# Optimization experiments

Hardware: AMD Instinct MI355X
Metric: run time of the kernel (lower is better)

## Reference

```python
import jax, jax.numpy as jnp
import numpy as np


def setup_inputs() -> dict:
    key = jax.random.key(0)
    k1, k2, k3, k4 = jax.random.split(key, 4)
    B, S, IN, OUT = 4, 2048, 4096, 11008
    x = jax.random.normal(k1, (B, S, IN), dtype=jnp.float32)
    # fp8-quantized weight values (simulated as small-magnitude floats stored in the param)
    weight = jax.random.normal(k2, (OUT, IN), dtype=jnp.float32)
    # per-output-channel dequant scale
    weight_scale = jax.random.uniform(k3, (OUT,), dtype=jnp.float32)
    bias = jax.random.normal(k4, (OUT,), dtype=jnp.float32)
    return {"x": x, "weight": weight, "weight_scale": weight_scale, "bias": bias}


def reference(x, weight, weight_scale, bias):
    # _dequant_weight: cast quantized weight to float32, broadcast per-row scale
    # (scale unsqueezed on trailing dims -> shape [out, 1]), multiply, cast to
    # compute dtype (x.dtype).
    compute_dtype = x.dtype
    q = weight.astype(jnp.float32)
    w = (q * weight_scale.astype(jnp.float32)[:, None]).astype(compute_dtype)  # [out, in]
    b = bias.astype(compute_dtype)
    # F.linear: y = x @ w.T + b
    y = jnp.einsum("bsi,oi->bso", x, w) + b
    return y
```

## Files before the change

### kernel.cpp

```cpp
#include <hip/hip_runtime.h>

#define M_DIM 8192
#define N_DIM 11008
#define K_DIM 4096
#define BM 256
#define BN 256
#define BK 64
#define NT (K_DIM / BK)
#define NIT (NT / 2)
#define TM (M_DIM / BM)
#define TN (N_DIM / BN)
#define NWG (TM * TN)

typedef __attribute__((ext_vector_type(8))) short bf16x8;
typedef __attribute__((ext_vector_type(8))) unsigned short u16x8;
typedef __attribute__((ext_vector_type(4))) float f32x4;

__device__ __forceinline__ unsigned short f2bf(float f) {
  union { float f; unsigned u; } v; v.f = f;
  unsigned r = v.u + 0x7FFFu + ((v.u >> 16) & 1u);
  return (unsigned short)(r >> 16);
}

__device__ __forceinline__ void gload_lds16(const unsigned short* g, unsigned short* l) {
  __builtin_amdgcn_global_load_lds(
      (const __attribute__((address_space(1))) void*)g,
      (__attribute__((address_space(3))) void*)l, 16, 0, 0);
}

__device__ __forceinline__ int swz(int b) { return b ^ (((b >> 7) & 7) << 4); }

#define BAR() asm volatile("s_barrier" ::: "memory")

__global__ void cvt_x_kernel(const float* __restrict__ in, unsigned short* __restrict__ o) {
  size_t i = (size_t)blockIdx.x * 256 + threadIdx.x;
  const float4* p = (const float4*)in + i * 2;
  float4 f0 = p[0], f1 = p[1];
  u16x8 v;
  v[0] = f2bf(f0.x); v[1] = f2bf(f0.y); v[2] = f2bf(f0.z); v[3] = f2bf(f0.w);
  v[4] = f2bf(f1.x); v[5] = f2bf(f1.y); v[6] = f2bf(f1.z); v[7] = f2bf(f1.w);
  *((u16x8*)o + i) = v;
}

__global__ void cvt_w_kernel(const float* __restrict__ in, const float* __restrict__ sc,
                             unsigned short* __restrict__ o) {
  size_t i = (size_t)blockIdx.x * 256 + threadIdx.x;
  float s = sc[i >> 9];
  const float4* p = (const float4*)in + i * 2;
  float4 f0 = p[0], f1 = p[1];
  u16x8 v;
  v[0] = f2bf(f0.x * s); v[1] = f2bf(f0.y * s); v[2] = f2bf(f0.z * s); v[3] = f2bf(f0.w * s);
  v[4] = f2bf(f1.x * s); v[5] = f2bf(f1.y * s); v[6] = f2bf(f1.z * s); v[7] = f2bf(f1.w * s);
  *((u16x8*)o + i) = v;
}

__launch_bounds__(512, 2)
__global__ void gemm_kernel(const unsigned short* __restrict__ xb,
                            const unsigned short* __restrict__ wb,
                            const float* __restrict__ bias,
                            float* __restrict__ out) {
  __shared__ unsigned short As[2][2][8192];
  __shared__ unsigned short Bs[2][2][8192];

  const int tid = threadIdx.x;
  const int lane = tid & 63;
  const int wave = tid >> 6;
  const int wr = wave >> 2;
  const int wc = wave & 3;

  int orig = blockIdx.x;
  int wg = (orig & 7) * (NWG / 8) + (orig >> 3);
  int bx = wg / TM;
  int by = wg % TM;
  const int rowBase = by * BM;
  const int colBase = bx * BN;

  f32x4 acc[8][4] = {};

  const int fr = lane & 15;
  const int q16 = (lane >> 4) * 16;

  float bias_v[4];
#pragma unroll
  for (int n = 0; n < 4; ++n)
    bias_v[n] = bias[colBase + wc * 64 + n * 16 + fr];

  const int L0 = tid * 16, L1 = L0 + 8192;
  const int S0 = swz(L0), S1 = swz(L1);
  const int sr0 = S0 >> 7, sc0_ = (S0 & 127) >> 1;
  const int sr1 = S1 >> 7, sc1_ = (S1 & 127) >> 1;

  auto stageA = [&](int kt, int half) {
    const unsigned short* src =
        xb + (size_t)(rowBase + half * 128) * K_DIM + (size_t)kt * BK;
    unsigned short* dst = &As[kt & 1][half][0];
    gload_lds16(src + (size_t)sr0 * K_DIM + sc0_, dst + (L0 >> 1));
    gload_lds16(src + (size_t)sr1 * K_DIM + sc1_, dst + (L1 >> 1));
  };
  auto stageB = [&](int kt, int half) {
    const unsigned short* src =
        wb + (size_t)(colBase + half * 128) * K_DIM + (size_t)kt * BK;
    unsigned short* dst = &Bs[kt & 1][half][0];
    gload_lds16(src + (size_t)sr0 * K_DIM + sc0_, dst + (L0 >> 1));
    gload_lds16(src + (size_t)sr1 * K_DIM + sc1_, dst + (L1 >> 1));
  };

  bf16x8 aF[8], bLo[4], bHi[4];

  auto rdA = [&](int d, int qm) {
    const char* Ab = (const char*)&As[d][wr][0];
#pragma unroll
    for (int mi = 0; mi < 4; ++mi)
#pragma unroll
      for (int ks = 0; ks < 2; ++ks) {
        int b = (qm * 64 + mi * 16 + fr) * 128 + ks * 64 + q16;
        aF[mi * 2 + ks] = *(const bf16x8*)(Ab + swz(b));
      }
  };
  auto rdB = [&](int d, int qn, bf16x8* bf) {
    const char* Bb = (const char*)&Bs[d][wc >> 1][0];
#pragma unroll
    for (int nj = 0; nj < 2; ++nj)
#pragma unroll
      for (int ks = 0; ks < 2; ++ks) {
        int b = ((wc & 1) * 64 + qn * 32 + nj * 16 + fr) * 128 + ks * 64 + q16;
        bf[nj * 2 + ks] = *(const bf16x8*)(Bb + swz(b));
      }
  };
  auto mma = [&](int qm, int qn, const bf16x8* bf) {
    __builtin_amdgcn_s_setprio(1);
#pragma unroll
    for (int mi = 0; mi < 4; ++mi)
#pragma unroll
      for (int nj = 0; nj < 2; ++nj)
#pragma unroll
        for (int ks = 0; ks < 2; ++ks)
          acc[qm * 4 + mi][qn * 2 + nj] = __builtin_amdgcn_mfma_f32_16x16x32_bf16(
              aF[mi * 2 + ks], bf[nj * 2 + ks], acc[qm * 4 + mi][qn * 2 + nj], 0, 0, 0);
    __builtin_amdgcn_s_setprio(0);
  };

  auto iter = [&](int a, bool f) {
    const int b = a + 1;
    rdA(0, 0); rdB(0, 0, bLo);
    stageA(b, 0);
    BAR(); mma(0, 0, bLo); BAR();
    rdB(0, 1, bHi);
    stageA(b, 1);
    BAR(); mma(0, 1, bHi); BAR();
    rdA(0, 1);
    if (f) stageB(a + 2, 0);
    BAR();
    mma(1, 1, bHi);
    if (f) stageB(a + 2, 1);
    mma(1, 0, bLo);
    if (f) { asm volatile("s_waitcnt vmcnt(4)" ::: "memory"); }
    else   { asm volatile("s_waitcnt vmcnt(0)" ::: "memory"); }
    BAR();
    rdA(1, 0); rdB(1, 0, bLo);
    if (f) stageA(a + 2, 0);
    BAR(); mma(0, 0, bLo); BAR();
    rdB(1, 1, bHi);
    if (f) stageA(a + 2, 1);
    BAR(); mma(0, 1, bHi); BAR();
    rdA(1, 1);
    if (f) stageB(a + 3, 0);
    BAR();
    mma(1, 1, bHi);
    if (f) stageB(a + 3, 1);
    mma(1, 0, bLo);
    if (f) { asm volatile("s_waitcnt vmcnt(4)" ::: "memory"); }
    BAR();
  };

  stageB(0, 0); stageB(0, 1);
  stageA(0, 0); stageA(0, 1);
  stageB(1, 0); stageB(1, 1);
  asm volatile("s_waitcnt vmcnt(4)" ::: "memory");
  BAR();

  for (int it = 0; it < NIT - 1; ++it) iter(2 * it, true);
  iter(NT - 2, false);

  const int r0 = (lane >> 4) * 4;
#pragma unroll
  for (int m = 0; m < 8; ++m) {
#pragma unroll
    for (int r = 0; r < 4; ++r) {
      size_t row = (size_t)(rowBase + wr * 128 + m * 16 + r0 + r);
      float* po = out + row * N_DIM + colBase + wc * 64 + fr;
#pragma unroll
      for (int n = 0; n < 4; ++n)
        po[n * 16] = acc[m][n][r] + bias_v[n];
    }
  }
}

extern "C" void kernel_launch(void* const* d_in, const int* in_sizes, int n_in,
                              void* d_out, int out_size, void* d_ws, size_t ws_size,
                              hipStream_t stream) {
  const float* x = (const float*)d_in[0];
  const float* w = (const float*)d_in[1];
  const float* sc = (const float*)d_in[2];
  const float* bi = (const float*)d_in[3];
  float* out = (float*)d_out;

  const size_t xe = (size_t)M_DIM * K_DIM;
  const size_t we = (size_t)N_DIM * K_DIM;
  unsigned short* xb = (unsigned short*)d_ws;
  unsigned short* wb = xb + xe;

  cvt_x_kernel<<<(unsigned)(xe / 8 / 256), 256, 0, stream>>>(x, xb);
  cvt_w_kernel<<<(unsigned)(we / 8 / 256), 256, 0, stream>>>(w, sc, wb);
  gemm_kernel<<<NWG, 512, 0, stream>>>(xb, wb, bi, out);
}
```

Measured before the change: 919.0 us.

## Software-pipeline LDS fragment reads with double register buffers across MFMA phases

Restructures the GEMM main loop so LDS fragment loads for the next quadrant are issued into separate register buffers (aP/aQ, bX/bY/bH) while MFMAs on the previous fragments run. Explicit lgkmcnt waits and sched_barrier fences pin the interleaving, and the last quadrant's MFMA is deferred into the next macro step. Global-to-LDS staging is redistributed with vmcnt(2) waits. The aim is to hide LDS read latency behind matrix work and drop some barriers, at the cost of more VGPR pressure under a 2-waves-per-SIMD launch bound and fragile hand-tuned wait counts.

```diff
diff --git a/kernel.cpp b/kernel.cpp
--- a/kernel.cpp
+++ b/kernel.cpp
@@ -7,7 +7,7 @@
 #define BN 256
 #define BK 64
 #define NT (K_DIM / BK)
-#define NIT (NT / 2)
+#define NMAC (NT / 2)
 #define TM (M_DIM / BM)
 #define TN (N_DIM / BN)
 #define NWG (TM * TN)
@@ -31,6 +31,7 @@
 __device__ __forceinline__ int swz(int b) { return b ^ (((b >> 7) & 7) << 4); }
 
 #define BAR() asm volatile("s_barrier" ::: "memory")
+#define SB0() __builtin_amdgcn_sched_barrier(0)
 
 __global__ void cvt_x_kernel(const float* __restrict__ in, unsigned short* __restrict__ o) {
   size_t i = (size_t)blockIdx.x * 256 + threadIdx.x;
@@ -105,29 +106,29 @@
     gload_lds16(src + (size_t)sr1 * K_DIM + sc1_, dst + (L1 >> 1));
   };
 
-  bf16x8 aF[8], bLo[4], bHi[4];
-
-  auto rdA = [&](int d, int qm) {
+  bf16x8 aP[8], aQ[8], bX[4], bY[4], bH[4];
+
+  auto rdA = [&](int d, int qm, bf16x8* dst) {
     const char* Ab = (const char*)&As[d][wr][0];
 #pragma unroll
     for (int mi = 0; mi < 4; ++mi)
 #pragma unroll
       for (int ks = 0; ks < 2; ++ks) {
         int b = (qm * 64 + mi * 16 + fr) * 128 + ks * 64 + q16;
-        aF[mi * 2 + ks] = *(const bf16x8*)(Ab + swz(b));
+        dst[mi * 2 + ks] = *(const bf16x8*)(Ab + swz(b));
       }
   };
-  auto rdB = [&](int d, int qn, bf16x8* bf) {
+  auto rdB = [&](int d, int qn, bf16x8* dst) {
     const char* Bb = (const char*)&Bs[d][wc >> 1][0];
 #pragma unroll
     for (int nj = 0; nj < 2; ++nj)
 #pragma unroll
       for (int ks = 0; ks < 2; ++ks) {
         int b = ((wc & 1) * 64 + qn * 32 + nj * 16 + fr) * 128 + ks * 64 + q16;
-        bf[nj * 2 + ks] = *(const bf16x8*)(Bb + swz(b));
+        dst[nj * 2 + ks] = *(const bf16x8*)(Bb + swz(b));
       }
   };
-  auto mma = [&](int qm, int qn, const bf16x8* bf) {
+  auto mma = [&](int qm, int qn, const bf16x8* A, const bf16x8* B) {
     __builtin_amdgcn_s_setprio(1);
 #pragma unroll
     for (int mi = 0; mi < 4; ++mi)
@@ -136,51 +137,69 @@
 #pragma unroll
         for (int ks = 0; ks < 2; ++ks)
           acc[qm * 4 + mi][qn * 2 + nj] = __builtin_amdgcn_mfma_f32_16x16x32_bf16(
-              aF[mi * 2 + ks], bf[nj * 2 + ks], acc[qm * 4 + mi][qn * 2 + nj], 0, 0, 0);
+              A[mi * 2 + ks], B[nj * 2 + ks], acc[qm * 4 + mi][qn * 2 + nj], 0, 0, 0);
     __builtin_amdgcn_s_setprio(0);
   };
 
-  auto iter = [&](int a, bool f) {
+  auto macro = [&](int a, bool first, bool notLast) {
     const int b = a + 1;
-    rdA(0, 0); rdB(0, 0, bLo);
-    stageA(b, 0);
-    BAR(); mma(0, 0, bLo); BAR();
-    rdB(0, 1, bHi);
+    const int da = a & 1, db = b & 1;
+    rdA(da, 0, aP); rdB(da, 0, bX);
     stageA(b, 1);
-    BAR(); mma(0, 1, bHi); BAR();
-    rdA(0, 1);
-    if (f) stageB(a + 2, 0);
-    BAR();
-    mma(1, 1, bHi);
-    if (f) stageB(a + 2, 1);
-    mma(1, 0, bLo);
-    if (f) { asm volatile("s_waitcnt vmcnt(4)" ::: "memory"); }
-    else   { asm volatile("s_waitcnt vmcnt(0)" ::: "memory"); }
-    BAR();
-    rdA(1, 0); rdB(1, 0, bLo);
-    if (f) stageA(a + 2, 0);
-    BAR(); mma(0, 0, bLo); BAR();
-    rdB(1, 1, bHi);
-    if (f) stageA(a + 2, 1);
-    BAR(); mma(0, 1, bHi); BAR();
-    rdA(1, 1);
-    if (f) stageB(a + 3, 0);
-    BAR();
-    mma(1, 1, bHi);
-    if (f) stageB(a + 3, 1);
-    mma(1, 0, bLo);
-    if (f) { asm volatile("s_waitcnt vmcnt(4)" ::: "memory"); }
-    BAR();
-  };
-
-  stageB(0, 0); stageB(0, 1);
-  stageA(0, 0); stageA(0, 1);
-  stageB(1, 0); stageB(1, 1);
-  asm volatile("s_waitcnt vmcnt(4)" ::: "memory");
+    if (!first) {
+      asm volatile("s_waitcnt lgkmcnt(12)" ::: "memory"); SB0();
+      mma(1, 0, aQ, bY);
+    }
+    BAR();
+    rdB(da, 1, bH);
+    stageB(b, 0);
+    asm volatile("s_waitcnt lgkmcnt(4)" ::: "memory"); SB0();
+    mma(0, 0, aP, bX);
+    BAR();
+    rdA(da, 1, aQ);
+    stageB(b, 1);
+    asm volatile("s_waitcnt lgkmcnt(8)" ::: "memory"); SB0();
+    mma(0, 1, aP, bH);
+    BAR();
+    if (notLast) stageA(a + 2, 0);
+    asm volatile("s_waitcnt lgkmcnt(0)" ::: "memory"); SB0();
+    mma(1, 1, aQ, bH);
+    if (notLast) { asm volatile("s_waitcnt vmcnt(2)" ::: "memory"); }
+    else         { asm volatile("s_waitcnt vmcnt(0)" ::: "memory"); }
+    BAR();
+    rdA(db, 0, aP); rdB(db, 0, bY);
+    if (notLast) stageA(a + 2, 1);
+    asm volatile("s_waitcnt lgkmcnt(12)" ::: "memory"); SB0();
+    mma(1, 0, aQ, bX);
+    BAR();
+    rdB(db, 1, bH);
+    if (notLast) stageB(a + 2, 0);
+    asm volatile("s_waitcnt lgkmcnt(4)" ::: "memory"); SB0();
+    mma(0, 0, aP, bY);
+    BAR();
+    rdA(db, 1, aQ);
+    if (notLast) stageB(a + 2, 1);
+    asm volatile("s_waitcnt lgkmcnt(8)" ::: "memory"); SB0();
+    mma(0, 1, aP, bH);
+    BAR();
+    if (notLast) stageA(b + 2, 0);
+    asm volatile("s_waitcnt lgkmcnt(0)" ::: "memory"); SB0();
+    mma(1, 1, aQ, bH);
+    if (notLast) { asm volatile("s_waitcnt vmcnt(2)" ::: "memory"); }
+    else         { asm volatile("s_waitcnt vmcnt(0)" ::: "memory"); }
+    BAR();
+  };
+
+  stageA(0, 0); stageA(0, 1); stageB(0, 0); stageB(0, 1);
+  stageA(1, 0);
+  asm volatile("s_waitcnt vmcnt(2)" ::: "memory");
   BAR();
 
-  for (int it = 0; it < NIT - 1; ++it) iter(2 * it, true);
-  iter(NT - 2, false);
+  macro(0, true, true);
+  for (int u = 1; u < NMAC - 1; ++u) macro(2 * u, false, true);
+  macro(2 * (NMAC - 1), false, false);
+  asm volatile("s_waitcnt lgkmcnt(0)" ::: "memory"); SB0();
+  mma(1, 0, aQ, bY);
 
   const int r0 = (lane >> 4) * 4;
 #pragma unroll
```

Result: slower. 2.006 ms (+118.2%).
